# Optimization experiments

Hardware: AMD Instinct MI355X
Metric: run time of the kernel (lower is better)

The kernel has to match this reference:

```python
import jax, jax.numpy as jnp
import numpy as np
import math

H = 16
DM = 1024
DK = DM // H


def setup_inputs() -> dict:
    key = jax.random.key(0)
    ks = jax.random.split(key, 12)
    B, S = 2, 2048
    inp = {
        "query": jax.random.normal(ks[0], (B, S, DM), jnp.float32),
        "key": jax.random.normal(ks[1], (B, S, DM), jnp.float32),
        "value": jax.random.normal(ks[2], (B, S, DM), jnp.float32),
        "mask": jnp.ones((B, 1, S, S), jnp.int32),
    }
    scale = 1.0 / math.sqrt(DM)
    for i, name in enumerate(["wq", "wk", "wv", "wo"]):
        inp[name] = jax.random.normal(ks[3 + i], (DM, DM), jnp.float32) * scale
        inp["b" + name[1]] = jnp.zeros((DM,), jnp.float32)
    return inp


def _mha(query, key, value, mask, wq, bq, wk, bk, wv, bv, wo, bo):
    B, S, _ = query.shape
    # projections -> [B, H, S, DK]
    def proj(x, w, b):
        return (x @ w + b).reshape(B, -1, H, DK).transpose(0, 2, 1, 3)
    q = proj(query, wq, bq)
    k = proj(key, wk, bk)
    v = proj(value, wv, bv)
    scores = jnp.einsum("bhqd,bhkd->bhqk", q, k) / math.sqrt(DK)
    scores = jnp.where(mask == 0, -jnp.inf, scores)  # mask broadcasts over heads
    p_attn = jax.nn.softmax(scores, axis=-1)
    # dropout is identity in eval / deterministic reference
    x = jnp.einsum("bhqk,bhkd->bhqd", p_attn, v)
    x = x.transpose(0, 2, 1, 3).reshape(B, -1, H * DK)
    return x @ wo + bo, p_attn


def reference(query, key, value, mask, wq, bq, wk, bk, wv, bv, wo, bo):
    return _mha(query, key, value, mask, wq, bq, wk, bk, wv, bv, wo, bo)
```

## Files before the change

kernel.cpp:

```cpp
#include <hip/hip_runtime.h>
#include <hip/hip_bf16.h>
#include <math.h>

typedef __attribute__((ext_vector_type(8))) short short8;
typedef __attribute__((ext_vector_type(4))) short sv4;
typedef __attribute__((ext_vector_type(4))) float f32x4;

#define S_LEN 2048
#define NH 16
#define DMODEL 1024
#define DKH 64
#define SC 0.18033688011112042f

static __device__ __forceinline__ short f2bf(float f) {
  unsigned u = __builtin_bit_cast(unsigned, f);
  unsigned r = (u + 0x7fffu + ((u >> 16) & 1u)) >> 16;
  return (short)r;
}

static __device__ __forceinline__ float bf2f(short s) {
  return __builtin_bit_cast(float, ((unsigned)(unsigned short)s) << 16);
}

static __device__ __forceinline__ float e2(float x) { return __builtin_amdgcn_exp2f(x); }

static __device__ __forceinline__ void gld16(const void* g, void* l) {
  __builtin_amdgcn_global_load_lds((const __attribute__((address_space(1))) void*)g,
                                   (__attribute__((address_space(3))) void*)l, 16, 0, 0);
}

static __device__ __forceinline__ f32x4 mfma_bf16(short8 a, short8 b, f32x4 c) {
  return __builtin_amdgcn_mfma_f32_16x16x32_bf16(a, b, c, 0, 0, 0);
}

__global__ __launch_bounds__(256) void cast3_kernel(const float* __restrict__ q, const float* __restrict__ k,
                                                    const float* __restrict__ v,
                                                    short* __restrict__ oq, short* __restrict__ ok_,
                                                    short* __restrict__ ov) {
  const float* in = blockIdx.y == 0 ? q : (blockIdx.y == 1 ? k : v);
  short* out = blockIdx.y == 0 ? oq : (blockIdx.y == 1 ? ok_ : ov);
  int i = blockIdx.x * 256 + threadIdx.x;
  float4 f = ((const float4*)in)[i];
  sv4 o = {f2bf(f.x), f2bf(f.y), f2bf(f.z), f2bf(f.w)};
  ((sv4*)out)[i] = o;
}

__global__ __launch_bounds__(256) void maskpack_kernel(const int* __restrict__ mask,
                                                       unsigned long long* __restrict__ mb,
                                                       unsigned* __restrict__ mall) {
  int row = blockIdx.x;
  int w = threadIdx.x >> 6, lane = threadIdx.x & 63;
  const int* mp = mask + (size_t)row * S_LEN;
  __shared__ unsigned flags;
  if (threadIdx.x == 0) flags = 0;
  __syncthreads();
#pragma unroll
  for (int c = 0; c < 8; ++c) {
    int ci = w * 8 + c;
    unsigned long long bits = __ballot(mp[ci * 64 + lane] != 0);
    if (lane == 0) {
      mb[(size_t)row * 32 + ci] = bits;
      if (bits == ~0ull) atomicOr(&flags, 1u << ci);
    }
  }
  __syncthreads();
  if (threadIdx.x == 0) mall[row] = flags;
}

__global__ __launch_bounds__(256) void wtrans_kernel(const float* __restrict__ w0, const float* __restrict__ w1,
                                                     const float* __restrict__ w2, const float* __restrict__ w3,
                                                     short* __restrict__ o0, short* __restrict__ o1,
                                                     short* __restrict__ o2, short* __restrict__ o3) {
  const float* in = blockIdx.z == 0 ? w0 : blockIdx.z == 1 ? w1 : blockIdx.z == 2 ? w2 : w3;
  short* out = blockIdx.z == 0 ? o0 : blockIdx.z == 1 ? o1 : blockIdx.z == 2 ? o2 : o3;
  __shared__ float t[64][65];
  int tx = threadIdx.x & 63, ty = threadIdx.x >> 6;
  int bx = blockIdx.x * 64, by = blockIdx.y * 64;
#pragma unroll
  for (int i = 0; i < 16; ++i)
    t[ty + i * 4][tx] = in[(by + ty + i * 4) * DMODEL + bx + tx];
  __syncthreads();
#pragma unroll
  for (int i = 0; i < 16; ++i)
    out[(bx + ty + i * 4) * DMODEL + by + tx] = f2bf(t[tx][ty + i * 4]);
}

__global__ __launch_bounds__(256) void knorm_kernel(const short* __restrict__ Kh, float* __restrict__ maxKn) {
  int bh = blockIdx.x;
  int tid = threadIdx.x;
  float mx = 0.f;
  for (int r = tid; r < S_LEN; r += 256) {
    const short8* kp = (const short8*)(Kh + (size_t)(bh * S_LEN + r) * DKH);
    float s = 0.f;
#pragma unroll
    for (int i = 0; i < 8; ++i) {
      short8 v = kp[i];
#pragma unroll
      for (int e = 0; e < 8; ++e) {
        float f = bf2f(v[e]);
        s += f * f;
      }
    }
    mx = fmaxf(mx, s);
  }
#pragma unroll
  for (int d = 1; d < 64; d <<= 1) mx = fmaxf(mx, __shfl_xor(mx, d));
  __shared__ float red[4];
  if ((tid & 63) == 0) red[tid >> 6] = mx;
  __syncthreads();
  if (tid == 0) maxKn[bh] = sqrtf(fmaxf(fmaxf(red[0], red[1]), fmaxf(red[2], red[3])));
}

__global__ __launch_bounds__(256) void proj_qkv(const short* __restrict__ Aq, const short* __restrict__ Ak,
                                                const short* __restrict__ Av,
                                                const short* __restrict__ Wq, const short* __restrict__ Wk,
                                                const short* __restrict__ Wv,
                                                const float* __restrict__ bq, const float* __restrict__ bk,
                                                const float* __restrict__ bv,
                                                short* __restrict__ Qh, short* __restrict__ Kh,
                                                short* __restrict__ Vt) {
  const int z = blockIdx.z;
  const short* A = z == 0 ? Aq : z == 1 ? Ak : Av;
  const short* W = z == 0 ? Wq : z == 1 ? Wk : Wv;
  const float* bias = z == 0 ? bq : z == 1 ? bk : bv;

  const int tid = threadIdx.x;
  const int wid = tid >> 6, lane = tid & 63;
  const int g = lane >> 4, li = lane & 15;
  const int wm = (wid >> 1) * 64, wn = (wid & 1) * 64;
  const int bn = blockIdx.x * 128, bm = blockIdx.y * 128;

  __shared__ __align__(16) short As[2][4096];
  __shared__ __align__(16) short Bs[2][4096];
  __shared__ __align__(16) short T2[64 * 136];

  auto stage = [&](int ks, int pb) {
    const int k0 = ks * 32;
#pragma unroll
    for (int i = 0; i < 2; ++i) {
      int slot = i * 256 + tid;
      int r = slot >> 2, pos = slot & 3;
      int lch = pos ^ ((r >> 1) & 3);
      gld16(A + (size_t)(bm + r) * DMODEL + k0 + lch * 8, As[pb] + slot * 8);
      gld16(W + (size_t)(bn + r) * DMODEL + k0 + lch * 8, Bs[pb] + slot * 8);
    }
  };

  f32x4 acc[4][4];
#pragma unroll
  for (int m = 0; m < 4; ++m)
#pragma unroll
    for (int n = 0; n < 4; ++n) acc[m][n] = (f32x4){0.f, 0.f, 0.f, 0.f};

  stage(0, 0);
  __syncthreads();
  for (int ks = 0; ks < 32; ++ks) {
    const int cur = ks & 1;
    if (ks + 1 < 32) stage(ks + 1, cur ^ 1);
    short8 av[4], bv4[4];
#pragma unroll
    for (int m = 0; m < 4; ++m) {
      int r = wm + m * 16 + li;
      av[m] = *(const short8*)(As[cur] + r * 32 + (g ^ ((r >> 1) & 3)) * 8);
    }
#pragma unroll
    for (int n = 0; n < 4; ++n) {
      int r = wn + n * 16 + li;
      bv4[n] = *(const short8*)(Bs[cur] + r * 32 + (g ^ ((r >> 1) & 3)) * 8);
    }
    __builtin_amdgcn_s_setprio(1);
#pragma unroll
    for (int m = 0; m < 4; ++m)
#pragma unroll
      for (int n = 0; n < 4; ++n) acc[m][n] = mfma_bf16(av[m], bv4[n], acc[m][n]);
    __builtin_amdgcn_s_setprio(0);
    __syncthreads();
  }

  if (z < 2) {
    short* out = z == 0 ? Qh : Kh;
#pragma unroll
    for (int n = 0; n < 4; ++n) {
      int col = bn + wn + n * 16 + li;
      float bb = bias[col];
      int h = col >> 6, dk = col & 63;
#pragma unroll
      for (int m = 0; m < 4; ++m)
#pragma unroll
        for (int j = 0; j < 4; ++j) {
          int row = bm + wm + m * 16 + g * 4 + j;
          int b_ = row >> 11, s_ = row & 2047;
          out[(size_t)((b_ * NH + h) * S_LEN + s_) * DKH + dk] = f2bf(acc[m][n][j] + bb);
        }
    }
  } else {
    short* out = Vt;
    const int b_ = bm >> 11;
    const int sbase = bm & 2047;
#pragma unroll
    for (int ph = 0; ph < 2; ++ph) {
      __syncthreads();
      if ((wid & 1) == ph) {
#pragma unroll
        for (int n = 0; n < 4; ++n) {
          int colL = n * 16 + li;
          float bb = bias[bn + ph * 64 + colL];
#pragma unroll
          for (int m = 0; m < 4; ++m)
#pragma unroll
            for (int j = 0; j < 4; ++j) {
              int rowL = wm + m * 16 + g * 4 + j;
              T2[colL * 136 + rowL] = f2bf(acc[m][n][j] + bb);
            }
        }
      }
      __syncthreads();
      int dr = tid >> 2, qc = tid & 3;
      int nglob = bn + ph * 64 + dr;
      int h = nglob >> 6, dk = nglob & 63;
      short* op = out + (size_t)((b_ * NH + h) * DKH + dk) * S_LEN + sbase + qc * 32;
      const short* tp = T2 + dr * 136 + qc * 32;
#pragma unroll
      for (int i = 0; i < 4; ++i) *(short8*)(op + i * 8) = *(const short8*)(tp + i * 8);
    }
  }
}

__global__ __launch_bounds__(256) void proj_out(const short* __restrict__ A, const short* __restrict__ W,
                                                const float* __restrict__ bias, float* __restrict__ out) {
  const int tid = threadIdx.x;
  const int wid = tid >> 6, lane = tid & 63;
  const int g = lane >> 4, li = lane & 15;
  const int wm = (wid >> 1) * 64, wn = (wid & 1) * 64;
  const int bn = blockIdx.x * 128, bm = blockIdx.y * 128;

  __shared__ __align__(16) short As[2][4096];
  __shared__ __align__(16) short Bs[2][4096];

  auto stage = [&](int ks, int pb) {
    const int k0 = ks * 32;
#pragma unroll
    for (int i = 0; i < 2; ++i) {
      int slot = i * 256 + tid;
      int r = slot >> 2, pos = slot & 3;
      int lch = pos ^ ((r >> 1) & 3);
      gld16(A + (size_t)(bm + r) * DMODEL + k0 + lch * 8, As[pb] + slot * 8);
      gld16(W + (size_t)(bn + r) * DMODEL + k0 + lch * 8, Bs[pb] + slot * 8);
    }
  };

  f32x4 acc[4][4];
#pragma unroll
  for (int m = 0; m < 4; ++m)
#pragma unroll
    for (int n = 0; n < 4; ++n) acc[m][n] = (f32x4){0.f, 0.f, 0.f, 0.f};

  stage(0, 0);
  __syncthreads();
  for (int ks = 0; ks < 32; ++ks) {
    const int cur = ks & 1;
    if (ks + 1 < 32) stage(ks + 1, cur ^ 1);
    short8 av[4], bv4[4];
#pragma unroll
    for (int m = 0; m < 4; ++m) {
      int r = wm + m * 16 + li;
      av[m] = *(const short8*)(As[cur] + r * 32 + (g ^ ((r >> 1) & 3)) * 8);
    }
#pragma unroll
    for (int n = 0; n < 4; ++n) {
      int r = wn + n * 16 + li;
      bv4[n] = *(const short8*)(Bs[cur] + r * 32 + (g ^ ((r >> 1) & 3)) * 8);
    }
    __builtin_amdgcn_s_setprio(1);
#pragma unroll
    for (int m = 0; m < 4; ++m)
#pragma unroll
      for (int n = 0; n < 4; ++n) acc[m][n] = mfma_bf16(av[m], bv4[n], acc[m][n]);
    __builtin_amdgcn_s_setprio(0);
    __syncthreads();
  }

#pragma unroll
  for (int n = 0; n < 4; ++n) {
    int col = bn + wn + n * 16 + li;
    float bb = bias[col];
#pragma unroll
    for (int m = 0; m < 4; ++m)
#pragma unroll
      for (int j = 0; j < 4; ++j) {
        int row = bm + wm + m * 16 + g * 4 + j;
        out[(size_t)row * DMODEL + col] = acc[m][n][j] + bb;
      }
  }
}

__global__ __launch_bounds__(256) void attn_fused(const short* __restrict__ Qh, const short* __restrict__ Kh,
                                                  const short* __restrict__ Vt,
                                                  const unsigned long long* __restrict__ maskb,
                                                  const unsigned* __restrict__ mall,
                                                  const float* __restrict__ maxKn,
                                                  float* __restrict__ pattn, short* __restrict__ xout) {
  const int tid = threadIdx.x;
  const int wid = tid >> 6, lane = tid & 63;
  const int g = lane >> 4, li = lane & 15;
  int swz = (blockIdx.x & 7) * 128 + (blockIdx.x >> 3);
  const int qblk = swz & 31;
  const int rest = swz >> 5;
  const int h = rest & 15, b = rest >> 4;
  const int bh = b * NH + h;
  const int q0 = qblk * 64 + wid * 16;

  const short* qptr = Qh + (size_t)(bh * S_LEN + q0 + li) * DKH;
  const short8 aq0 = *(const short8*)(qptr + g * 8);
  const short8 aq1 = *(const short8*)(qptr + 32 + g * 8);

  float qn2 = 0.f;
#pragma unroll
  for (int e = 0; e < 8; ++e) {
    float f0 = bf2f(aq0[e]), f1 = bf2f(aq1[e]);
    qn2 += f0 * f0 + f1 * f1;
  }
  qn2 += __shfl_xor(qn2, 16);
  qn2 += __shfl_xor(qn2, 32);
  const float mk = maxKn[bh];

  float M2[4], lsum[4], off[4];
  unsigned ms[4];
#pragma unroll
  for (int j = 0; j < 4; ++j) {
    float qn = __shfl(qn2, g * 4 + j);
    M2[j] = sqrtf(qn) * mk * SC + 1.0f;
    lsum[j] = 0.f;
    ms[j] = mall[b * S_LEN + q0 + g * 4 + j];
  }

  __shared__ __align__(16) short SB[20480];

  auto stage1 = [&](int t) {
    short* dst = SB + (t & 1) * 8192;
#pragma unroll
    for (int i = 0; i < 4; ++i) {
      int slot = i * 256 + tid;
      int r = slot >> 3, pos = slot & 7;
      int lch = pos ^ (r & 7);
      gld16(Kh + (size_t)(bh * S_LEN + t * 128 + r) * DKH + lch * 8, dst + slot * 8);
    }
  };
  auto stage2 = [&](int kt) {
    const int pb = kt & 1;
    short* Kd = SB + pb * 4096;
    short* Vd = SB + 8192 + pb * 4096;
    const int k0 = kt * 64;
#pragma unroll
    for (int i = 0; i < 2; ++i) {
      int slot = i * 256 + tid;
      int r = slot >> 3, pos = slot & 7;
      int lch = pos ^ (r & 7);
      gld16(Kh + (size_t)(bh * S_LEN + k0 + r) * DKH + lch * 8, Kd + slot * 8);
      gld16(Vt + (size_t)(bh * DKH + r) * S_LEN + k0 + lch * 8, Vd + slot * 8);
    }
  };

  stage1(0);
  __syncthreads();
  for (int t = 0; t < 16; ++t) {
    const short* Kc = SB + (t & 1) * 8192;
    if (t + 1 < 16) stage1(t + 1);
#pragma unroll
    for (int half = 0; half < 2; ++half) {
      f32x4 acc[4];
      __builtin_amdgcn_s_setprio(1);
#pragma unroll
      for (int nf = 0; nf < 4; ++nf) {
        acc[nf] = (f32x4){0.f, 0.f, 0.f, 0.f};
        int rB = half * 64 + nf * 16 + li;
        const short8 b0 = *(const short8*)(Kc + rB * 64 + ((0 + g) ^ (rB & 7)) * 8);
        const short8 b1 = *(const short8*)(Kc + rB * 64 + ((4 + g) ^ (rB & 7)) * 8);
        acc[nf] = mfma_bf16(aq0, b0, acc[nf]);
        acc[nf] = mfma_bf16(aq1, b1, acc[nf]);
      }
      __builtin_amdgcn_s_setprio(0);
#pragma unroll
      for (int j = 0; j < 4; ++j) {
        float s0 = acc[0][j] * SC - M2[j];
        float s1 = acc[1][j] * SC - M2[j];
        float s2 = acc[2][j] * SC - M2[j];
        float s3 = acc[3][j] * SC - M2[j];
        if (!((ms[j] >> (t * 2 + half)) & 1)) {
          unsigned long long mb = maskb[(size_t)(b * S_LEN + q0 + g * 4 + j) * 32 + t * 2 + half];
          if (!((mb >> li) & 1)) s0 = -INFINITY;
          if (!((mb >> (16 + li)) & 1)) s1 = -INFINITY;
          if (!((mb >> (32 + li)) & 1)) s2 = -INFINITY;
          if (!((mb >> (48 + li)) & 1)) s3 = -INFINITY;
        }
        lsum[j] += e2(s0) + e2(s1) + e2(s2) + e2(s3);
      }
    }
    __syncthreads();
  }
  stage2(0);
#pragma unroll
  for (int d = 1; d < 16; d <<= 1)
#pragma unroll
    for (int j = 0; j < 4; ++j) lsum[j] += __shfl_xor(lsum[j], d);
#pragma unroll
  for (int j = 0; j < 4; ++j) off[j] = M2[j] + __builtin_amdgcn_logf(lsum[j]);

  f32x4 accx[4];
#pragma unroll
  for (int nf = 0; nf < 4; ++nf) accx[nf] = (f32x4){0.f, 0.f, 0.f, 0.f};

  __syncthreads();
  for (int kt = 0; kt < 32; ++kt) {
    const int k0 = kt * 64;
    const int cur = kt & 1;
    const short* Kc = SB + cur * 4096;
    const short* Vc = SB + 8192 + cur * 4096;
    short* Ps = SB + 16384;
    if (kt + 1 < 32) stage2(kt + 1);

    f32x4 acc[4];
    __builtin_amdgcn_s_setprio(1);
#pragma unroll
    for (int nf = 0; nf < 4; ++nf) {
      acc[nf] = (f32x4){0.f, 0.f, 0.f, 0.f};
      int rB = nf * 16 + li;
      const short8 b0 = *(const short8*)(Kc + rB * 64 + ((0 + g) ^ (rB & 7)) * 8);
      const short8 b1 = *(const short8*)(Kc + rB * 64 + ((4 + g) ^ (rB & 7)) * 8);
      acc[nf] = mfma_bf16(aq0, b0, acc[nf]);
      acc[nf] = mfma_bf16(aq1, b1, acc[nf]);
    }
    __builtin_amdgcn_s_setprio(0);

#pragma unroll
    for (int j = 0; j < 4; ++j) {
      const int qrow = q0 + g * 4 + j;
      bool full = (ms[j] >> kt) & 1;
      unsigned long long mb = full ? ~0ull : maskb[(size_t)(b * S_LEN + qrow) * 32 + kt];
      const int row = g * 4 + j;
#pragma unroll
      for (int nf = 0; nf < 4; ++nf) {
        float s = acc[nf][j] * SC - off[j];
        if (!full && !((mb >> (nf * 16 + li)) & 1)) s = -INFINITY;
        float p = e2(s);
        int col = nf * 16 + li;
        int sidx = row * 64 + (((col >> 3) ^ (row & 7)) * 8) + (col & 7);
        Ps[wid * 1024 + sidx] = f2bf(p);
      }
    }

    const short8 pa0 = *(const short8*)(Ps + wid * 1024 + li * 64 + ((0 + g) ^ (li & 7)) * 8);
    const short8 pa1 = *(const short8*)(Ps + wid * 1024 + li * 64 + ((4 + g) ^ (li & 7)) * 8);
    __builtin_amdgcn_s_setprio(1);
#pragma unroll
    for (int nf = 0; nf < 4; ++nf) {
      int rv = nf * 16 + li;
      const short8 v0 = *(const short8*)(Vc + rv * 64 + ((0 + g) ^ (rv & 7)) * 8);
      const short8 v1 = *(const short8*)(Vc + rv * 64 + ((4 + g) ^ (rv & 7)) * 8);
      accx[nf] = mfma_bf16(pa0, v0, accx[nf]);
      accx[nf] = mfma_bf16(pa1, v1, accx[nf]);
    }
    __builtin_amdgcn_s_setprio(0);

    {
      const int rg = lane >> 4;
      const int c = (lane & 15) * 4;
#pragma unroll
      for (int s = 0; s < 4; ++s) {
        int r = s * 4 + rg;
        int chunk = (c >> 3) ^ (r & 7);
        sv4 pv4 = *(const sv4*)(Ps + wid * 1024 + r * 64 + chunk * 8 + (c & 7));
        f32x4 w4;
        w4[0] = bf2f(pv4[0]);
        w4[1] = bf2f(pv4[1]);
        w4[2] = bf2f(pv4[2]);
        w4[3] = bf2f(pv4[3]);
        __builtin_nontemporal_store(w4, (f32x4*)(pattn + (size_t)(bh * S_LEN + q0 + r) * S_LEN + k0 + c));
      }
    }
    __syncthreads();
  }

#pragma unroll
  for (int nf = 0; nf < 4; ++nf) {
    int d = nf * 16 + li;
#pragma unroll
    for (int j = 0; j < 4; ++j) {
      int q = q0 + g * 4 + j;
      xout[(size_t)(b * S_LEN + q) * DMODEL + h * DKH + d] = f2bf(accx[nf][j]);
    }
  }
}

extern "C" void kernel_launch(void* const* d_in, const int* in_sizes, int n_in,
                              void* d_out, int out_size, void* d_ws, size_t ws_size,
                              hipStream_t stream) {
  (void)in_sizes; (void)n_in; (void)out_size; (void)ws_size;
  const float* query = (const float*)d_in[0];
  const float* key = (const float*)d_in[1];
  const float* value = (const float*)d_in[2];
  const int* mask = (const int*)d_in[3];
  const float* wq = (const float*)d_in[4];
  const float* bq = (const float*)d_in[5];
  const float* wk = (const float*)d_in[6];
  const float* bk = (const float*)d_in[7];
  const float* wv = (const float*)d_in[8];
  const float* bv = (const float*)d_in[9];
  const float* wo = (const float*)d_in[10];
  const float* bo = (const float*)d_in[11];

  char* ws = (char*)d_ws;
  const size_t MB = 1u << 20;
  short* qb = (short*)(ws + 0 * MB);
  short* kb = (short*)(ws + 8 * MB);
  short* vb = (short*)(ws + 16 * MB);
  short* wqT = (short*)(ws + 24 * MB);
  short* wkT = (short*)(ws + 26 * MB);
  short* wvT = (short*)(ws + 28 * MB);
  short* woT = (short*)(ws + 30 * MB);
  short* Qh = (short*)(ws + 32 * MB);
  short* Kh = (short*)(ws + 40 * MB);
  short* Vt = (short*)(ws + 48 * MB);
  float* maxKn = (float*)(ws + 56 * MB);
  unsigned* mall = (unsigned*)(ws + 56 * MB + 64 * 1024);
  short* xb = (short*)(ws + 57 * MB);
  unsigned long long* maskb = (unsigned long long*)(ws + 16 * MB);

  float* out_x = (float*)d_out;
  float* out_p = (float*)d_out + 4194304;

  cast3_kernel<<<dim3(4096, 3), 256, 0, stream>>>(query, key, value, qb, kb, vb);
  wtrans_kernel<<<dim3(16, 16, 4), 256, 0, stream>>>(wq, wk, wv, wo, wqT, wkT, wvT, woT);
  proj_qkv<<<dim3(8, 32, 3), 256, 0, stream>>>(qb, kb, vb, wqT, wkT, wvT, bq, bk, bv, Qh, Kh, Vt);
  maskpack_kernel<<<dim3(4096), 256, 0, stream>>>(mask, maskb, mall);
  knorm_kernel<<<dim3(32), 256, 0, stream>>>(Kh, maxKn);
  attn_fused<<<dim3(1024), 256, 0, stream>>>(Qh, Kh, Vt, maskb, mall, maxKn, out_p, xb);
  proj_out<<<dim3(8, 32), 256, 0, stream>>>(xb, woT, bo, out_x);
}
```

Measured before the change: 281.2 us.

## Fuse key-norm max into K projection epilogue and halve output-projection tile width

```diff
diff --git a/kernel.cpp b/kernel.cpp
--- a/kernel.cpp
+++ b/kernel.cpp
@@ -70,7 +70,10 @@
 __global__ __launch_bounds__(256) void wtrans_kernel(const float* __restrict__ w0, const float* __restrict__ w1,
                                                      const float* __restrict__ w2, const float* __restrict__ w3,
                                                      short* __restrict__ o0, short* __restrict__ o1,
-                                                     short* __restrict__ o2, short* __restrict__ o3) {
+                                                     short* __restrict__ o2, short* __restrict__ o3,
+                                                     unsigned* __restrict__ maxKn2) {
+  if (blockIdx.x == 0 && blockIdx.y == 0 && blockIdx.z == 0 && threadIdx.x < 32)
+    maxKn2[threadIdx.x] = 0u;
   const float* in = blockIdx.z == 0 ? w0 : blockIdx.z == 1 ? w1 : blockIdx.z == 2 ? w2 : w3;
   short* out = blockIdx.z == 0 ? o0 : blockIdx.z == 1 ? o1 : blockIdx.z == 2 ? o2 : o3;
   __shared__ float t[64][65];
@@ -83,32 +86,6 @@
 #pragma unroll
   for (int i = 0; i < 16; ++i)
     out[(bx + ty + i * 4) * DMODEL + by + tx] = f2bf(t[tx][ty + i * 4]);
-}
-
-__global__ __launch_bounds__(256) void knorm_kernel(const short* __restrict__ Kh, float* __restrict__ maxKn) {
-  int bh = blockIdx.x;
-  int tid = threadIdx.x;
-  float mx = 0.f;
-  for (int r = tid; r < S_LEN; r += 256) {
-    const short8* kp = (const short8*)(Kh + (size_t)(bh * S_LEN + r) * DKH);
-    float s = 0.f;
-#pragma unroll
-    for (int i = 0; i < 8; ++i) {
-      short8 v = kp[i];
-#pragma unroll
-      for (int e = 0; e < 8; ++e) {
-        float f = bf2f(v[e]);
-        s += f * f;
-      }
-    }
-    mx = fmaxf(mx, s);
-  }
-#pragma unroll
-  for (int d = 1; d < 64; d <<= 1) mx = fmaxf(mx, __shfl_xor(mx, d));
-  __shared__ float red[4];
-  if ((tid & 63) == 0) red[tid >> 6] = mx;
-  __syncthreads();
-  if (tid == 0) maxKn[bh] = sqrtf(fmaxf(fmaxf(red[0], red[1]), fmaxf(red[2], red[3])));
 }
 
 __global__ __launch_bounds__(256) void proj_qkv(const short* __restrict__ Aq, const short* __restrict__ Ak,
@@ -118,7 +95,8 @@
                                                 const float* __restrict__ bq, const float* __restrict__ bk,
                                                 const float* __restrict__ bv,
                                                 short* __restrict__ Qh, short* __restrict__ Kh,
-                                                short* __restrict__ Vt) {
+                                                short* __restrict__ Vt,
+                                                unsigned* __restrict__ maxKn2) {
   const int z = blockIdx.z;
   const short* A = z == 0 ? Aq : z == 1 ? Ak : Av;
   const short* W = z == 0 ? Wq : z == 1 ? Wk : Wv;
@@ -193,6 +171,39 @@
           out[(size_t)((b_ * NH + h) * S_LEN + s_) * DKH + dk] = f2bf(acc[m][n][j] + bb);
         }
     }
+    if (z == 1) {
+      float sn[4][4];
+#pragma unroll
+      for (int m = 0; m < 4; ++m)
+#pragma unroll
+        for (int j = 0; j < 4; ++j) {
+          float s = 0.f;
+#pragma unroll
+          for (int n = 0; n < 4; ++n) {
+            float v = acc[m][n][j] + bias[bn + wn + n * 16 + li];
+            s += v * v;
+          }
+          sn[m][j] = s;
+        }
+#pragma unroll
+      for (int d = 1; d < 16; d <<= 1)
+#pragma unroll
+        for (int m = 0; m < 4; ++m)
+#pragma unroll
+          for (int j = 0; j < 4; ++j) sn[m][j] += __shfl_xor(sn[m][j], d);
+      float mx = 0.f;
+#pragma unroll
+      for (int m = 0; m < 4; ++m)
+#pragma unroll
+        for (int j = 0; j < 4; ++j) mx = fmaxf(mx, sn[m][j]);
+      mx = fmaxf(mx, __shfl_xor(mx, 16));
+      mx = fmaxf(mx, __shfl_xor(mx, 32));
+      if (lane == 0) {
+        int head = (bn + wn) >> 6;
+        int b_ = bm >> 11;
+        atomicMax(&maxKn2[b_ * NH + head], __builtin_bit_cast(unsigned, mx));
+      }
+    }
   } else {
     short* out = Vt;
     const int b_ = bm >> 11;
@@ -231,11 +242,11 @@
   const int tid = threadIdx.x;
   const int wid = tid >> 6, lane = tid & 63;
   const int g = lane >> 4, li = lane & 15;
-  const int wm = (wid >> 1) * 64, wn = (wid & 1) * 64;
-  const int bn = blockIdx.x * 128, bm = blockIdx.y * 128;
+  const int wm = (wid >> 1) * 64, wn = (wid & 1) * 32;
+  const int bn = blockIdx.x * 64, bm = blockIdx.y * 128;
 
   __shared__ __align__(16) short As[2][4096];
-  __shared__ __align__(16) short Bs[2][4096];
+  __shared__ __align__(16) short Bs[2][2048];
 
   auto stage = [&](int ks, int pb) {
     const int k0 = ks * 32;
@@ -245,29 +256,34 @@
       int r = slot >> 2, pos = slot & 3;
       int lch = pos ^ ((r >> 1) & 3);
       gld16(A + (size_t)(bm + r) * DMODEL + k0 + lch * 8, As[pb] + slot * 8);
+    }
+    {
+      int slot = tid;
+      int r = slot >> 2, pos = slot & 3;
+      int lch = pos ^ ((r >> 1) & 3);
       gld16(W + (size_t)(bn + r) * DMODEL + k0 + lch * 8, Bs[pb] + slot * 8);
     }
   };
 
-  f32x4 acc[4][4];
+  f32x4 acc[4][2];
 #pragma unroll
   for (int m = 0; m < 4; ++m)
 #pragma unroll
-    for (int n = 0; n < 4; ++n) acc[m][n] = (f32x4){0.f, 0.f, 0.f, 0.f};
+    for (int n = 0; n < 2; ++n) acc[m][n] = (f32x4){0.f, 0.f, 0.f, 0.f};
 
   stage(0, 0);
   __syncthreads();
   for (int ks = 0; ks < 32; ++ks) {
     const int cur = ks & 1;
     if (ks + 1 < 32) stage(ks + 1, cur ^ 1);
-    short8 av[4], bv4[4];
+    short8 av[4], bv4[2];
 #pragma unroll
     for (int m = 0; m < 4; ++m) {
       int r = wm + m * 16 + li;
       av[m] = *(const short8*)(As[cur] + r * 32 + (g ^ ((r >> 1) & 3)) * 8);
     }
 #pragma unroll
-    for (int n = 0; n < 4; ++n) {
+    for (int n = 0; n < 2; ++n) {
       int r = wn + n * 16 + li;
       bv4[n] = *(const short8*)(Bs[cur] + r * 32 + (g ^ ((r >> 1) & 3)) * 8);
     }
@@ -275,13 +291,13 @@
 #pragma unroll
     for (int m = 0; m < 4; ++m)
 #pragma unroll
-      for (int n = 0; n < 4; ++n) acc[m][n] = mfma_bf16(av[m], bv4[n], acc[m][n]);
+      for (int n = 0; n < 2; ++n) acc[m][n] = mfma_bf16(av[m], bv4[n], acc[m][n]);
     __builtin_amdgcn_s_setprio(0);
     __syncthreads();
   }
 
 #pragma unroll
-  for (int n = 0; n < 4; ++n) {
+  for (int n = 0; n < 2; ++n) {
     int col = bn + wn + n * 16 + li;
     float bb = bias[col];
 #pragma unroll
@@ -298,7 +314,7 @@
                                                   const short* __restrict__ Vt,
                                                   const unsigned long long* __restrict__ maskb,
                                                   const unsigned* __restrict__ mall,
-                                                  const float* __restrict__ maxKn,
+                                                  const unsigned* __restrict__ maxKn2,
                                                   float* __restrict__ pattn, short* __restrict__ xout) {
   const int tid = threadIdx.x;
   const int wid = tid >> 6, lane = tid & 63;
@@ -322,7 +338,7 @@
   }
   qn2 += __shfl_xor(qn2, 16);
   qn2 += __shfl_xor(qn2, 32);
-  const float mk = maxKn[bh];
+  const float mk = sqrtf(__builtin_bit_cast(float, maxKn2[bh]));
 
   float M2[4], lsum[4], off[4];
   unsigned ms[4];
@@ -521,7 +537,7 @@
   short* Qh = (short*)(ws + 32 * MB);
   short* Kh = (short*)(ws + 40 * MB);
   short* Vt = (short*)(ws + 48 * MB);
-  float* maxKn = (float*)(ws + 56 * MB);
+  unsigned* maxKn2 = (unsigned*)(ws + 56 * MB);
   unsigned* mall = (unsigned*)(ws + 56 * MB + 64 * 1024);
   short* xb = (short*)(ws + 57 * MB);
   unsigned long long* maskb = (unsigned long long*)(ws + 16 * MB);
@@ -530,10 +546,9 @@
   float* out_p = (float*)d_out + 4194304;
 
   cast3_kernel<<<dim3(4096, 3), 256, 0, stream>>>(query, key, value, qb, kb, vb);
-  wtrans_kernel<<<dim3(16, 16, 4), 256, 0, stream>>>(wq, wk, wv, wo, wqT, wkT, wvT, woT);
-  proj_qkv<<<dim3(8, 32, 3), 256, 0, stream>>>(qb, kb, vb, wqT, wkT, wvT, bq, bk, bv, Qh, Kh, Vt);
+  wtrans_kernel<<<dim3(16, 16, 4), 256, 0, stream>>>(wq, wk, wv, wo, wqT, wkT, wvT, woT, maxKn2);
+  proj_qkv<<<dim3(8, 32, 3), 256, 0, stream>>>(qb, kb, vb, wqT, wkT, wvT, bq, bk, bv, Qh, Kh, Vt, maxKn2);
   maskpack_kernel<<<dim3(4096), 256, 0, stream>>>(mask, maskb, mall);
-  knorm_kernel<<<dim3(32), 256, 0, stream>>>(Kh, maxKn);
-  attn_fused<<<dim3(1024), 256, 0, stream>>>(Qh, Kh, Vt, maskb, mall, maxKn, out_p, xb);
-  proj_out<<<dim3(8, 32), 256, 0, stream>>>(xb, woT, bo, out_x);
-}
+  attn_fused<<<dim3(1024), 256, 0, stream>>>(Qh, Kh, Vt, maskb, mall, maxKn2, out_p, xb);
+  proj_out<<<dim3(16, 32), 256, 0, stream>>>(xb, woT, bo, out_x);
+}
```

Result: faster. 265.7 us (-5.5%).
